# Kernel tuning notes

Hardware: AMD Instinct MI355X
Metric: run time of the kernel (lower is better)

Reference implementation:

```python
import jax, jax.numpy as jnp
import numpy as np

EPS = 1e-8


def setup_inputs() -> dict:
    key = jax.random.key(0)
    k1, k2, k3, k4 = jax.random.split(key, 4)
    B, N, M, C = 512, 512, 128, 1024
    addr = M + 6  # read head: k(M) + beta(1) + g(1) + s(3) + gamma(1)
    controller_out = jax.random.normal(k1, (B, C), dtype=jnp.float32)
    prev_w = jax.random.uniform(k2, (B, N), dtype=jnp.float32)
    prev_w = prev_w / prev_w.sum(axis=1, keepdims=True)  # valid weighting
    memory_state = jax.random.normal(k3, (B, N, M), dtype=jnp.float32)
    W_fc = jax.random.normal(k4, (C, addr), dtype=jnp.float32) * 0.02
    b_fc = jnp.zeros((addr,), dtype=jnp.float32)
    return {"controller_out": controller_out, "prev_w": prev_w,
            "memory_state": memory_state, "W_fc": W_fc, "b_fc": b_fc}


def reference(controller_out, prev_w, memory_state, W_fc, b_fc):
    M = memory_state.shape[2]
    out = controller_out @ W_fc + b_fc  # [B, M+6]
    k = out[:, :M]                                   # key
    beta = jax.nn.softplus(out[:, M:M + 1])          # key strength
    g = jax.nn.sigmoid(out[:, M + 1:M + 2])          # interpolation gate
    s = jax.nn.softmax(out[:, M + 2:M + 5], axis=1)  # 3-tap shift weights
    gamma = 1.0 + jax.nn.softplus(out[:, M + 5:M + 6])

    # Content addressing (Eq. 5-6): cosine similarity + sharpened softmax
    norm_k = jnp.linalg.norm(k, axis=1, keepdims=True) + EPS      # [B,1]
    norm_mem = jnp.linalg.norm(memory_state, axis=2) + EPS        # [B,N]
    sim = jnp.einsum('bnm,bm->bn', memory_state, k) / (norm_k * norm_mem)
    w_c = jax.nn.softmax(beta * sim, axis=1)

    # Interpolation (Eq. 7)
    w_g = g * w_c + (1.0 - g) * prev_w

    # Circular 3-tap shift (Eq. 8): vectorized roll instead of per-slot loop
    w_s = (s[:, 0:1] * jnp.roll(w_g, 1, axis=1)
           + s[:, 1:2] * w_g
           + s[:, 2:3] * jnp.roll(w_g, -1, axis=1))

    # Sharpening (Eq. 9)
    w_pow = w_s ** gamma
    w = w_pow / (w_pow.sum(axis=1, keepdims=True) + EPS)

    # Read vector (read head)
    read_vec = jnp.einsum('bn,bnm->bm', w, memory_state)
    return (read_vec, w)
```

## Files before the change

kernel.cpp:

```cpp
#include <hip/hip_runtime.h>
#include <math.h>

#define BB   512
#define NN   512
#define MM   128
#define CC   1024
#define ADDR 134
#define EPSF 1e-8f

__device__ __forceinline__ float softplus_f(float x) {
    return fmaxf(x, 0.0f) + log1pf(expf(-fabsf(x)));
}

__global__ __launch_bounds__(1024, 8) void ntm_head_kernel(
    const float* __restrict__ co,
    const float* __restrict__ prev_w,
    const float* __restrict__ mem,
    const float* __restrict__ W_fc,
    const float* __restrict__ b_fc,
    float* __restrict__ out_rv,
    float* __restrict__ out_w)
{
    __shared__ __align__(16) float s_co[CC];
    __shared__ __align__(16) float s_k[MM];
    __shared__ float s_extra[8];
    __shared__ __align__(16) float s_bsim[NN];
    __shared__ float s_wg[NN];
    __shared__ float s_w[NN];
    __shared__ __align__(16) float s_part[32 * MM];
    __shared__ float s_red[16];
    __shared__ float s_params[8];

    const int t = threadIdx.x;
    const int b = blockIdx.x;
    const int gi = t >> 5;
    const int l  = t & 31;
    const float4* memb = (const float4*)(mem + (size_t)b * NN * MM);

    s_co[t] = co[(size_t)b * CC + t];
    float pw = (t < NN) ? prev_w[(size_t)b * NN + t] : 0.0f;
    __syncthreads();

    {
        const int o    = t & (MM - 1);
        const int part = t >> 7;
        const float* Wp = W_fc + o;
        float a0 = 0.f, a1 = 0.f, a2 = 0.f, a3 = 0.f;
        const int c0 = part * (CC / 8);
        for (int c = c0; c < c0 + CC / 8; c += 4) {
            float4 cv = *(const float4*)(s_co + c);
            a0 = fmaf(cv.x, Wp[(size_t)(c + 0) * ADDR], a0);
            a1 = fmaf(cv.y, Wp[(size_t)(c + 1) * ADDR], a1);
            a2 = fmaf(cv.z, Wp[(size_t)(c + 2) * ADDR], a2);
            a3 = fmaf(cv.w, Wp[(size_t)(c + 3) * ADDR], a3);
        }
        s_part[part * MM + o] = (a0 + a1) + (a2 + a3);

        const int wv = t >> 6;
        if (wv < 6) {
            const int ll = t & 63;
            const int oe = MM + wv;
            const float* We = W_fc + oe;
            float e = 0.f;
            for (int c = ll; c < CC; c += 64)
                e = fmaf(s_co[c], We[(size_t)c * ADDR], e);
            #pragma unroll
            for (int off = 32; off >= 1; off >>= 1) e += __shfl_xor(e, off, 64);
            if (ll == 0) s_extra[wv] = e + b_fc[oe];
        }
    }

    float4 p0 = memb[(size_t)(gi      ) * 32 + l];
    float4 p1 = memb[(size_t)(gi + 32 ) * 32 + l];
    float4 p2 = memb[(size_t)(gi + 64 ) * 32 + l];
    float4 p3 = memb[(size_t)(gi + 96 ) * 32 + l];

    __syncthreads();

    if (t < MM) {
        float r = b_fc[t];
        #pragma unroll
        for (int p = 0; p < 8; ++p) r += s_part[p * MM + t];
        s_k[t] = r;
        float v = r * r;
        #pragma unroll
        for (int off = 32; off >= 1; off >>= 1) v += __shfl_xor(v, off, 64);
        if ((t & 63) == 0) s_red[t >> 6] = v;
    }
    __syncthreads();
    if (t == 0) {
        float ks = s_red[0] + s_red[1];
        float norm_k = sqrtf(ks) + EPSF;
        float beta = softplus_f(s_extra[0]);
        float g = 1.0f / (1.0f + expf(-s_extra[1]));
        float e0 = s_extra[2], e1 = s_extra[3], e2 = s_extra[4];
        float mx = fmaxf(e0, fmaxf(e1, e2));
        float x0 = expf(e0 - mx), x1 = expf(e1 - mx), x2 = expf(e2 - mx);
        float inv = 1.0f / (x0 + x1 + x2);
        s_params[0] = beta / norm_k;
        s_params[1] = g;
        s_params[2] = x0 * inv;
        s_params[3] = x1 * inv;
        s_params[4] = x2 * inv;
        s_params[5] = 1.0f + softplus_f(s_extra[5]);
    }
    __syncthreads();

    const float bnk = s_params[0];
    const float4 kv = ((const float4*)s_k)[l];

    #pragma unroll
    for (int j = 0; j < 16; j += 4) {
        float4 a0 = p0, a1 = p1, a2 = p2, a3 = p3;
        if (j + 4 < 16) {
            p0 = memb[(size_t)(gi + (j + 4) * 32) * 32 + l];
            p1 = memb[(size_t)(gi + (j + 5) * 32) * 32 + l];
            p2 = memb[(size_t)(gi + (j + 6) * 32) * 32 + l];
            p3 = memb[(size_t)(gi + (j + 7) * 32) * 32 + l];
        }
        float d0 = a0.x*kv.x + a0.y*kv.y + a0.z*kv.z + a0.w*kv.w;
        float q0 = a0.x*a0.x + a0.y*a0.y + a0.z*a0.z + a0.w*a0.w;
        float d1 = a1.x*kv.x + a1.y*kv.y + a1.z*kv.z + a1.w*kv.w;
        float q1 = a1.x*a1.x + a1.y*a1.y + a1.z*a1.z + a1.w*a1.w;
        float d2 = a2.x*kv.x + a2.y*kv.y + a2.z*kv.z + a2.w*kv.w;
        float q2 = a2.x*a2.x + a2.y*a2.y + a2.z*a2.z + a2.w*a2.w;
        float d3 = a3.x*kv.x + a3.y*kv.y + a3.z*kv.z + a3.w*kv.w;
        float q3 = a3.x*a3.x + a3.y*a3.y + a3.z*a3.z + a3.w*a3.w;
        #pragma unroll
        for (int off = 16; off >= 1; off >>= 1) {
            d0 += __shfl_xor(d0, off, 64); q0 += __shfl_xor(q0, off, 64);
            d1 += __shfl_xor(d1, off, 64); q1 += __shfl_xor(q1, off, 64);
            d2 += __shfl_xor(d2, off, 64); q2 += __shfl_xor(q2, off, 64);
            d3 += __shfl_xor(d3, off, 64); q3 += __shfl_xor(q3, off, 64);
        }
        float dd = d0, qq = q0; int rr = gi + j * 32;
        if (l == 1) { dd = d1; qq = q1; rr = gi + (j + 1) * 32; }
        if (l == 2) { dd = d2; qq = q2; rr = gi + (j + 2) * 32; }
        if (l == 3) { dd = d3; qq = q3; rr = gi + (j + 3) * 32; }
        if (l < 4) s_bsim[rr] = bnk * dd / (sqrtf(qq) + EPSF);
    }

    p0 = memb[(size_t)(gi      ) * 32 + l];
    p1 = memb[(size_t)(gi + 32 ) * 32 + l];
    p2 = memb[(size_t)(gi + 64 ) * 32 + l];
    p3 = memb[(size_t)(gi + 96 ) * 32 + l];

    __syncthreads();

    {
        const float NEG = -3.0e38f;
        float b1 = (t < NN) ? s_bsim[t] : NEG;

        float m = b1;
        #pragma unroll
        for (int off = 32; off >= 1; off >>= 1) m = fmaxf(m, __shfl_xor(m, off, 64));
        if ((t & 63) == 0) s_red[t >> 6] = m;
        __syncthreads();
        float M8 = s_red[0];
        #pragma unroll
        for (int i = 1; i < 8; ++i) M8 = fmaxf(M8, s_red[i]);
        __syncthreads();

        float e1 = (t < NN) ? expf(b1 - M8) : 0.0f;
        float ls = e1;
        #pragma unroll
        for (int off = 32; off >= 1; off >>= 1) ls += __shfl_xor(ls, off, 64);
        if ((t & 63) == 0) s_red[t >> 6] = ls;
        __syncthreads();
        float S = s_red[0];
        #pragma unroll
        for (int i = 1; i < 8; ++i) S += s_red[i];
        __syncthreads();

        const float invS = 1.0f / S;
        const float g = s_params[1];
        float wg1 = fmaf(g, e1 * invS, (1.0f - g) * pw);
        if (t < NN) s_wg[t] = wg1;
        __syncthreads();

        const float sh0 = s_params[2], sh1 = s_params[3], sh2 = s_params[4];
        const float gamma = s_params[5];
        float wp1 = 0.0f;
        if (t < NN) {
            float ws1 = sh0 * s_wg[(t + NN - 1) & (NN - 1)]
                      + sh1 * wg1
                      + sh2 * s_wg[(t + 1) & (NN - 1)];
            wp1 = powf(ws1, gamma);
        }
        float lz = wp1;
        #pragma unroll
        for (int off = 32; off >= 1; off >>= 1) lz += __shfl_xor(lz, off, 64);
        if ((t & 63) == 0) s_red[t >> 6] = lz;
        __syncthreads();
        float Z = s_red[0];
        #pragma unroll
        for (int i = 1; i < 8; ++i) Z += s_red[i];
        __syncthreads();

        const float invZ = 1.0f / (Z + EPSF);
        if (t < NN) {
            float w1 = wp1 * invZ;
            s_w[t] = w1;
            out_w[(size_t)b * NN + t] = w1;
        }
    }
    __syncthreads();

    {
        float4 acc = make_float4(0.f, 0.f, 0.f, 0.f);
        #pragma unroll
        for (int j = 0; j < 16; j += 4) {
            float4 a0 = p0, a1 = p1, a2 = p2, a3 = p3;
            const int r0 = gi + (j    ) * 32;
            const int r1 = gi + (j + 1) * 32;
            const int r2 = gi + (j + 2) * 32;
            const int r3 = gi + (j + 3) * 32;
            if (j + 4 < 16) {
                p0 = memb[(size_t)(gi + (j + 4) * 32) * 32 + l];
                p1 = memb[(size_t)(gi + (j + 5) * 32) * 32 + l];
                p2 = memb[(size_t)(gi + (j + 6) * 32) * 32 + l];
                p3 = memb[(size_t)(gi + (j + 7) * 32) * 32 + l];
            }
            float w0 = s_w[r0], w1 = s_w[r1], w2 = s_w[r2], w3 = s_w[r3];
            acc.x = fmaf(w0, a0.x, acc.x); acc.y = fmaf(w0, a0.y, acc.y);
            acc.z = fmaf(w0, a0.z, acc.z); acc.w = fmaf(w0, a0.w, acc.w);
            acc.x = fmaf(w1, a1.x, acc.x); acc.y = fmaf(w1, a1.y, acc.y);
            acc.z = fmaf(w1, a1.z, acc.z); acc.w = fmaf(w1, a1.w, acc.w);
            acc.x = fmaf(w2, a2.x, acc.x); acc.y = fmaf(w2, a2.y, acc.y);
            acc.z = fmaf(w2, a2.z, acc.z); acc.w = fmaf(w2, a2.w, acc.w);
            acc.x = fmaf(w3, a3.x, acc.x); acc.y = fmaf(w3, a3.y, acc.y);
            acc.z = fmaf(w3, a3.z, acc.z); acc.w = fmaf(w3, a3.w, acc.w);
        }
        *((float4*)&s_part[gi * MM + l * 4]) = acc;
        __syncthreads();

        if (t < 512) {
            const int h = t >> 7;
            const int o = t & (MM - 1);
            float r = 0.f;
            #pragma unroll
            for (int q = 0; q < 8; ++q) r += s_part[(h * 8 + q) * MM + o];
            s_bsim[h * MM + o] = r;
        }
        __syncthreads();
        if (t < MM) {
            float r = s_bsim[t] + s_bsim[MM + t] + s_bsim[2 * MM + t] + s_bsim[3 * MM + t];
            out_rv[(size_t)b * MM + t] = r;
        }
    }
}

extern "C" void kernel_launch(void* const* d_in, const int* in_sizes, int n_in,
                              void* d_out, int out_size, void* d_ws, size_t ws_size,
                              hipStream_t stream) {
    const float* co     = (const float*)d_in[0];
    const float* prev_w = (const float*)d_in[1];
    const float* mem    = (const float*)d_in[2];
    const float* W_fc   = (const float*)d_in[3];
    const float* b_fc   = (const float*)d_in[4];
    float* out = (float*)d_out;
    ntm_head_kernel<<<BB, 1024, 0, stream>>>(co, prev_w, mem, W_fc, b_fc,
                                             out, out + (size_t)BB * MM);
}
```

Before: 228.8 us.

## Keep memory rows in registers across passes and use transpose-style shuffle reduction

Each thread now loads all 16 of its memory float4 chunks once into registers, up front, and precomputes squared norms there. Both the similarity pass and the read-vector pass reuse those registers, so memory_state is read from global memory once instead of twice. The eight separate butterfly reductions are replaced by a transpose-style shuffle that packs dot products and norms into fewer shuffles. Launch bounds drop to 4 waves per SIMD to give room for the larger register footprint, which lowers occupancy.

```diff
diff --git a/kernel.cpp b/kernel.cpp
--- a/kernel.cpp
+++ b/kernel.cpp
@@ -12,7 +12,7 @@
     return fmaxf(x, 0.0f) + log1pf(expf(-fabsf(x)));
 }
 
-__global__ __launch_bounds__(1024, 8) void ntm_head_kernel(
+__global__ __launch_bounds__(1024, 4) void ntm_head_kernel(
     const float* __restrict__ co,
     const float* __restrict__ prev_w,
     const float* __restrict__ mem,
@@ -70,17 +70,21 @@
         }
     }
 
-    float4 p0 = memb[(size_t)(gi      ) * 32 + l];
-    float4 p1 = memb[(size_t)(gi + 32 ) * 32 + l];
-    float4 p2 = memb[(size_t)(gi + 64 ) * 32 + l];
-    float4 p3 = memb[(size_t)(gi + 96 ) * 32 + l];
+    float4 p[16];
+    float qq[16];
+    #pragma unroll
+    for (int jj = 0; jj < 16; ++jj) {
+        p[jj] = memb[(size_t)gi * 32 + l + (size_t)jj * 1024];
+        qq[jj] = p[jj].x * p[jj].x + p[jj].y * p[jj].y
+               + p[jj].z * p[jj].z + p[jj].w * p[jj].w;
+    }
 
     __syncthreads();
 
     if (t < MM) {
         float r = b_fc[t];
         #pragma unroll
-        for (int p = 0; p < 8; ++p) r += s_part[p * MM + t];
+        for (int q = 0; q < 8; ++q) r += s_part[q * MM + t];
         s_k[t] = r;
         float v = r * r;
         #pragma unroll
@@ -111,40 +115,34 @@
 
     #pragma unroll
     for (int j = 0; j < 16; j += 4) {
-        float4 a0 = p0, a1 = p1, a2 = p2, a3 = p3;
-        if (j + 4 < 16) {
-            p0 = memb[(size_t)(gi + (j + 4) * 32) * 32 + l];
-            p1 = memb[(size_t)(gi + (j + 5) * 32) * 32 + l];
-            p2 = memb[(size_t)(gi + (j + 6) * 32) * 32 + l];
-            p3 = memb[(size_t)(gi + (j + 7) * 32) * 32 + l];
-        }
-        float d0 = a0.x*kv.x + a0.y*kv.y + a0.z*kv.z + a0.w*kv.w;
-        float q0 = a0.x*a0.x + a0.y*a0.y + a0.z*a0.z + a0.w*a0.w;
-        float d1 = a1.x*kv.x + a1.y*kv.y + a1.z*kv.z + a1.w*kv.w;
-        float q1 = a1.x*a1.x + a1.y*a1.y + a1.z*a1.z + a1.w*a1.w;
-        float d2 = a2.x*kv.x + a2.y*kv.y + a2.z*kv.z + a2.w*kv.w;
-        float q2 = a2.x*a2.x + a2.y*a2.y + a2.z*a2.z + a2.w*a2.w;
-        float d3 = a3.x*kv.x + a3.y*kv.y + a3.z*kv.z + a3.w*kv.w;
-        float q3 = a3.x*a3.x + a3.y*a3.y + a3.z*a3.z + a3.w*a3.w;
-        #pragma unroll
-        for (int off = 16; off >= 1; off >>= 1) {
-            d0 += __shfl_xor(d0, off, 64); q0 += __shfl_xor(q0, off, 64);
-            d1 += __shfl_xor(d1, off, 64); q1 += __shfl_xor(q1, off, 64);
-            d2 += __shfl_xor(d2, off, 64); q2 += __shfl_xor(q2, off, 64);
-            d3 += __shfl_xor(d3, off, 64); q3 += __shfl_xor(q3, off, 64);
-        }
-        float dd = d0, qq = q0; int rr = gi + j * 32;
-        if (l == 1) { dd = d1; qq = q1; rr = gi + (j + 1) * 32; }
-        if (l == 2) { dd = d2; qq = q2; rr = gi + (j + 2) * 32; }
-        if (l == 3) { dd = d3; qq = q3; rr = gi + (j + 3) * 32; }
-        if (l < 4) s_bsim[rr] = bnk * dd / (sqrtf(qq) + EPSF);
-    }
-
-    p0 = memb[(size_t)(gi      ) * 32 + l];
-    p1 = memb[(size_t)(gi + 32 ) * 32 + l];
-    p2 = memb[(size_t)(gi + 64 ) * 32 + l];
-    p3 = memb[(size_t)(gi + 96 ) * 32 + l];
-
+        float d0 = p[j  ].x*kv.x + p[j  ].y*kv.y + p[j  ].z*kv.z + p[j  ].w*kv.w;
+        float d1 = p[j+1].x*kv.x + p[j+1].y*kv.y + p[j+1].z*kv.z + p[j+1].w*kv.w;
+        float d2 = p[j+2].x*kv.x + p[j+2].y*kv.y + p[j+2].z*kv.z + p[j+2].w*kv.w;
+        float d3 = p[j+3].x*kv.x + p[j+3].y*kv.y + p[j+3].z*kv.z + p[j+3].w*kv.w;
+        float q0 = qq[j], q1 = qq[j+1], q2 = qq[j+2], q3 = qq[j+3];
+
+        d0 += __shfl_xor(d0, 16, 64); q0 += __shfl_xor(q0, 16, 64);
+        d1 += __shfl_xor(d1, 16, 64); q1 += __shfl_xor(q1, 16, 64);
+        d2 += __shfl_xor(d2, 16, 64); q2 += __shfl_xor(q2, 16, 64);
+        d3 += __shfl_xor(d3, 16, 64); q3 += __shfl_xor(q3, 16, 64);
+        float W0 = (l & 16) ? q0 : d0;
+        float W1 = (l & 16) ? q1 : d1;
+        float W2 = (l & 16) ? q2 : d2;
+        float W3 = (l & 16) ? q3 : d3;
+        W0 += __shfl_xor(W0, 8, 64); W1 += __shfl_xor(W1, 8, 64);
+        W2 += __shfl_xor(W2, 8, 64); W3 += __shfl_xor(W3, 8, 64);
+        float X0 = (l & 8) ? W1 : W0;
+        float X1 = (l & 8) ? W3 : W2;
+        X0 += __shfl_xor(X0, 4, 64); X1 += __shfl_xor(X1, 4, 64);
+        float Y = (l & 4) ? X1 : X0;
+        Y += __shfl_xor(Y, 2, 64);
+        Y += __shfl_xor(Y, 1, 64);
+        float Q = __shfl_xor(Y, 16, 64);
+        if (l < 16 && (l & 3) == 0) {
+            int jj = j + ((l & 4) >> 1) + ((l & 8) >> 3);
+            s_bsim[gi + jj * 32] = bnk * Y / (sqrtf(Q) + EPSF);
+        }
+    }
     __syncthreads();
 
     {
@@ -209,27 +207,12 @@
     {
         float4 acc = make_float4(0.f, 0.f, 0.f, 0.f);
         #pragma unroll
-        for (int j = 0; j < 16; j += 4) {
-            float4 a0 = p0, a1 = p1, a2 = p2, a3 = p3;
-            const int r0 = gi + (j    ) * 32;
-            const int r1 = gi + (j + 1) * 32;
-            const int r2 = gi + (j + 2) * 32;
-            const int r3 = gi + (j + 3) * 32;
-            if (j + 4 < 16) {
-                p0 = memb[(size_t)(gi + (j + 4) * 32) * 32 + l];
-                p1 = memb[(size_t)(gi + (j + 5) * 32) * 32 + l];
-                p2 = memb[(size_t)(gi + (j + 6) * 32) * 32 + l];
-                p3 = memb[(size_t)(gi + (j + 7) * 32) * 32 + l];
-            }
-            float w0 = s_w[r0], w1 = s_w[r1], w2 = s_w[r2], w3 = s_w[r3];
-            acc.x = fmaf(w0, a0.x, acc.x); acc.y = fmaf(w0, a0.y, acc.y);
-            acc.z = fmaf(w0, a0.z, acc.z); acc.w = fmaf(w0, a0.w, acc.w);
-            acc.x = fmaf(w1, a1.x, acc.x); acc.y = fmaf(w1, a1.y, acc.y);
-            acc.z = fmaf(w1, a1.z, acc.z); acc.w = fmaf(w1, a1.w, acc.w);
-            acc.x = fmaf(w2, a2.x, acc.x); acc.y = fmaf(w2, a2.y, acc.y);
-            acc.z = fmaf(w2, a2.z, acc.z); acc.w = fmaf(w2, a2.w, acc.w);
-            acc.x = fmaf(w3, a3.x, acc.x); acc.y = fmaf(w3, a3.y, acc.y);
-            acc.z = fmaf(w3, a3.z, acc.z); acc.w = fmaf(w3, a3.w, acc.w);
+        for (int jj = 0; jj < 16; ++jj) {
+            float w = s_w[gi + jj * 32];
+            acc.x = fmaf(w, p[jj].x, acc.x);
+            acc.y = fmaf(w, p[jj].y, acc.y);
+            acc.z = fmaf(w, p[jj].z, acc.z);
+            acc.w = fmaf(w, p[jj].w, acc.w);
         }
         *((float4*)&s_part[gi * MM + l * 4]) = acc;
         __syncthreads();
```

After: 233.2 us. No clear change (+1.9%).
